# Performance work log

Hardware: AMD Instinct MI355X
Metric: run time of the kernel (lower is better)

Reference implementation:

```python
import jax, jax.numpy as jnp
import numpy as np

HEADS = 16
NEG_INF = np.float32(-2**32 + 1)  # matches TF code's padding value


def setup_inputs() -> dict:
    key = jax.random.key(0)
    ks = jax.random.split(key, 11)
    B, S, D = 2, 2048, 1024
    mk = lambda k, shape: jax.random.normal(k, shape, dtype=jnp.float32)
    return {
        "query": mk(ks[0], (B, S, D)),
        "key":   mk(ks[1], (B, S, D)),
        "value": mk(ks[2], (B, S, D)),
        "Wq": mk(ks[3], (D, D)) * (1.0 / np.sqrt(D)), "bq": jnp.zeros((D,), jnp.float32),
        "Wk": mk(ks[4], (D, D)) * (1.0 / np.sqrt(D)), "bk": jnp.zeros((D,), jnp.float32),
        "Wv": mk(ks[5], (D, D)) * (1.0 / np.sqrt(D)), "bv": jnp.zeros((D,), jnp.float32),
        "Wo": mk(ks[6], (D, D)) * (1.0 / np.sqrt(D)), "bo": jnp.zeros((D,), jnp.float32),
    }


def reference(query, key, value, Wq, bq, Wk, bk, Wv, bv, Wo, bo):
    B, S, D = query.shape
    H = HEADS
    dh = D // H
    # QKV projections with relu (as in the original Dense(activation=relu))
    q = jax.nn.relu(query @ Wq + bq).reshape(B, S, H, dh)
    k = jax.nn.relu(key   @ Wk + bk).reshape(B, S, H, dh)
    v = jax.nn.relu(value @ Wv + bv).reshape(B, S, H, dh)
    # scaled dot-product attention; scale = sqrt(per-head key dim)
    scores = jnp.einsum("bqhd,bkhd->bhqk", q, k) / jnp.sqrt(jnp.float32(dh))
    # causal mask (masked=True path): zeros above the diagonal -> NEG_INF
    causal = jnp.tril(jnp.ones((S, S), dtype=jnp.float32))  # [S,S]
    scores = jnp.where(causal == 0, NEG_INF, scores)
    attn = jax.nn.softmax(scores, axis=-1)  # [B,H,S,S]
    out = jnp.einsum("bhqk,bkhd->bqhd", attn, v).reshape(B, S, D)
    return jax.nn.relu(out @ Wo + bo)
```

## Files before the change

### kernel.cpp

```cpp
#include <hip/hip_runtime.h>
#include <hip/hip_bf16.h>

using bf16 = __hip_bfloat16;
typedef __attribute__((ext_vector_type(8))) short bf16x8;
typedef __attribute__((ext_vector_type(4))) float f32x4;

#define DEV __device__ __forceinline__

DEV float exp2fast(float x) { return __builtin_amdgcn_exp2f(x); }

DEV void gload_lds16(const void* g, void* l) {
  __builtin_amdgcn_global_load_lds((const __attribute__((address_space(1))) void*)g,
                                   (__attribute__((address_space(3))) void*)l, 16, 0, 0);
}

DEV unsigned pk2(float lo, float hi) {
  union { bf16 h[2]; unsigned u; } z;
  z.h[0] = __float2bfloat16(lo);
  z.h[1] = __float2bfloat16(hi);
  return z.u;
}

struct PrepArgs {
  const float* x[3]; bf16* y[3];
  const float* W[4]; bf16* WT[4];
};

__global__ __launch_bounds__(256) void prep_kernel(PrepArgs a) {
  __shared__ float tile[32][33];
  const int b = blockIdx.x;
  if (b < 6144) {
    const int which = b >> 11, blk = b & 2047;
    const int i = blk * 256 + threadIdx.x;
    const float4* xv = (const float4*)a.x[which];
    float4 p = xv[i * 2];
    float4 q = xv[i * 2 + 1];
    union { bf16 h[8]; uint4 v; } u;
    u.h[0] = __float2bfloat16(p.x); u.h[1] = __float2bfloat16(p.y);
    u.h[2] = __float2bfloat16(p.z); u.h[3] = __float2bfloat16(p.w);
    u.h[4] = __float2bfloat16(q.x); u.h[5] = __float2bfloat16(q.y);
    u.h[6] = __float2bfloat16(q.z); u.h[7] = __float2bfloat16(q.w);
    *(uint4*)&a.y[which][(size_t)i * 8] = u.v;
  } else {
    const int w = (b - 6144) >> 10, blk = (b - 6144) & 1023;
    const float* W = a.W[w];
    bf16* WT = a.WT[w];
    const int tx = threadIdx.x & 31, ty = threadIdx.x >> 5;
    const int n0 = (blk & 31) * 32, k0 = (blk >> 5) * 32;
#pragma unroll
    for (int i = ty; i < 32; i += 8)
      tile[i][tx] = W[(size_t)(k0 + i) * 1024 + n0 + tx];
    __syncthreads();
#pragma unroll
    for (int i = ty; i < 32; i += 8)
      WT[(size_t)(n0 + i) * 1024 + k0 + tx] = __float2bfloat16(tile[tx][i]);
  }
}

__global__ __launch_bounds__(256) void vtrans_kernel(const bf16* __restrict__ v,
                                                     bf16* __restrict__ VT) {
  __shared__ bf16 tile[64 * 64];
  const int t = threadIdx.x;
  const int bh = blockIdx.y, b = bh >> 4, h = bh & 15;
  const int s0 = blockIdx.x * 64;
  const int r0 = t >> 3, c8 = t & 7;
#pragma unroll
  for (int it = 0; it < 2; ++it) {
    int r = it * 32 + r0;
    uint4 d = *(const uint4*)&v[(size_t)(b * 2048 + s0 + r) * 1024 + h * 64 + c8 * 8];
    *(uint4*)&tile[r * 64 + ((c8 ^ (r >> 3)) * 8)] = d;
  }
  __syncthreads();
#pragma unroll
  for (int it = 0; it < 2; ++it) {
    int d = it * 32 + r0;
    int sc = c8 * 8;
    union { bf16 h[8]; uint4 v4; } u;
#pragma unroll
    for (int j = 0; j < 8; ++j) {
      int row = sc + j;
      u.h[j] = tile[row * 64 + (((d >> 3) ^ (row >> 3)) * 8) + (d & 7)];
    }
    *(uint4*)&VT[((size_t)bh * 64 + d) * 2048 + s0 + sc] = u.v4;
  }
}

template <int BM, typename OutT>
DEV void gemm_core(const bf16* __restrict__ A, const bf16* __restrict__ BT,
                   const float* __restrict__ bias, OutT* __restrict__ out) {
  constexpr int K = 1024, N = 1024;
  constexpr int MI = BM / 32;
  __shared__ bf16 ldsA[2][BM * 32];
  __shared__ bf16 ldsB[2][128 * 32];
  const int t = threadIdx.x;
  const int lane = t & 63, wid = t >> 6;
  const int wr = wid >> 1, wc = wid & 1;
  const int fr = lane & 15, fko = (lane >> 4) * 8;
  const size_t mBase = (size_t)blockIdx.y * BM;
  const size_t nBase = (size_t)blockIdx.x * 128;

  const int srow = t >> 2;
  const int scol = (t & 3) * 8;
  const bf16* gA = A + (mBase + srow) * K + scol;
  const bf16* gB = BT + (nBase + srow) * K + scol;
  const int ldst = wid * 512;

  f32x4 acc[MI][4];
#pragma unroll
  for (int i = 0; i < MI; ++i)
#pragma unroll
    for (int j = 0; j < 4; ++j) acc[i][j] = (f32x4){0.f, 0.f, 0.f, 0.f};

  gload_lds16(gA, &ldsA[0][ldst]);
  if constexpr (BM == 128) gload_lds16(gA + 64 * K, &ldsA[0][ldst + 2048]);
  gload_lds16(gB, &ldsB[0][ldst]);
  gload_lds16(gB + 64 * K, &ldsB[0][ldst + 2048]);
  __syncthreads();

  int buf = 0;
  for (int k0 = 0; k0 < K; k0 += 32) {
    if (k0 + 32 < K) {
      const int kn = k0 + 32;
      gload_lds16(gA + kn, &ldsA[buf ^ 1][ldst]);
      if constexpr (BM == 128) gload_lds16(gA + 64 * K + kn, &ldsA[buf ^ 1][ldst + 2048]);
      gload_lds16(gB + kn, &ldsB[buf ^ 1][ldst]);
      gload_lds16(gB + 64 * K + kn, &ldsB[buf ^ 1][ldst + 2048]);
    }
    bf16x8 aF[MI], bF[4];
#pragma unroll
    for (int i = 0; i < MI; ++i)
      aF[i] = *(const bf16x8*)&ldsA[buf][(wr * (BM / 2) + i * 16 + fr) * 32 + fko];
#pragma unroll
    for (int j = 0; j < 4; ++j)
      bF[j] = *(const bf16x8*)&ldsB[buf][(wc * 64 + j * 16 + fr) * 32 + fko];
#pragma unroll
    for (int i = 0; i < MI; ++i)
#pragma unroll
      for (int j = 0; j < 4; ++j)
        acc[i][j] = __builtin_amdgcn_mfma_f32_16x16x32_bf16(aF[i], bF[j], acc[i][j], 0, 0, 0);
    __syncthreads();
    buf ^= 1;
  }

  const int orow = (int)mBase + wr * (BM / 2) + (lane >> 4) * 4;
  const int ocol = (int)nBase + wc * 64 + fr;
#pragma unroll
  for (int j = 0; j < 4; ++j) {
    const float bj = bias[ocol + j * 16];
#pragma unroll
    for (int i = 0; i < MI; ++i)
#pragma unroll
      for (int r = 0; r < 4; ++r) {
        float v = fmaxf(acc[i][j][r] + bj, 0.f);
        size_t idx = (size_t)(orow + i * 16 + r) * N + (ocol + j * 16);
        if constexpr (sizeof(OutT) == 2) out[idx] = __float2bfloat16(v);
        else out[idx] = v;
      }
  }
}

struct QKVArgs {
  const bf16* A[3];
  const bf16* BT[3];
  const float* bias[3];
  bf16* out[3];
};

__global__ __launch_bounds__(256) void gemm_qkv_kernel(QKVArgs args) {
  const int z = blockIdx.z;
  gemm_core<128, bf16>(args.A[z], args.BT[z], args.bias[z], args.out[z]);
}

__global__ __launch_bounds__(256) void gemm_out_kernel(const bf16* __restrict__ A,
                                                       const bf16* __restrict__ BT,
                                                       const float* __restrict__ bias,
                                                       float* __restrict__ out) {
  gemm_core<64, float>(A, BT, bias, out);
}

__global__ __launch_bounds__(256, 2) void attn_kernel(const bf16* __restrict__ Qb,
                                                      const bf16* __restrict__ Kb,
                                                      const bf16* __restrict__ VTb,
                                                      bf16* __restrict__ Ob) {
  constexpr int Dm = 1024, S = 2048;
  __shared__ bf16 ldsK[2][128 * 64];
  __shared__ bf16 ldsV[2][64 * 128];
  const int t = threadIdx.x, l = t & 63, wid = t >> 6;

  const int lin = blockIdx.y * 16 + blockIdx.x;
  const int swz = (lin & 7) * 64 + (lin >> 3);
  const int bh = swz >> 4, pairp = swz & 15;
  const int b = bh >> 4, h = bh & 15;
  const int q4 = l & 15, fg = l >> 4;
  const bf16* Qg = Qb + (size_t)b * S * Dm + h * 64;
  const bf16* Kg = Kb + (size_t)b * S * Dm + h * 64;
  const bf16* VTg = VTb + (size_t)bh * 64 * S;

  const int krow0 = wid * 32 + (l >> 3);
  const int kch = ((l & 7) ^ (l >> 3)) * 8;
  const int vrl = l >> 4;
  const int vcb = l & 15;

  const int idx0 = ((q4 + ((l & 16) ? 32 : 0)) << 2);
  const int idx1 = idx0 + 64;

  constexpr float SC = 0.18033688f;

  auto STAGE = [&](int tile, int bi) {
    const int kvb = tile * 128;
#pragma unroll
    for (int g = 0; g < 4; ++g)
      gload_lds16(Kg + (size_t)(kvb + krow0 + 8 * g) * Dm + kch,
                  &ldsK[bi][(wid * 32 + 8 * g) * 64]);
#pragma unroll
    for (int g = 0; g < 4; ++g) {
      const int dr = wid * 16 + 4 * g + vrl;
      const int vch = (vcb ^ (4 * g + vrl)) * 8;
      gload_lds16(VTg + (size_t)dr * S + kvb + vch,
                  &ldsV[bi][(wid * 16 + 4 * g) * 128]);
    }
  };

#pragma unroll 1
  for (int ph = 0; ph < 2; ++ph) {
    const int qt = ph ? (31 - pairp) : pairp;
    const int qb = qt * 64;
    const int qw = qb + wid * 16;

    bf16x8 qF[2];
#pragma unroll
    for (int kd = 0; kd < 2; ++kd)
      qF[kd] = *(const bf16x8*)&Qg[(size_t)(qw + q4) * Dm + kd * 32 + fg * 8];

    f32x4 oacc[4];
#pragma unroll
    for (int n = 0; n < 4; ++n) oacc[n] = (f32x4){0.f, 0.f, 0.f, 0.f};
    float mrow = -3.0e38f, lsum = 0.f;

    const int nTiles = (qt + 2) >> 1;

    STAGE(0, 0);
    __syncthreads();

    int buf = 0;
    for (int tile = 0; tile < nTiles; ++tile) {
      const int kvb = tile * 128;
      if (tile + 1 < nTiles) STAGE(tile + 1, buf ^ 1);
      const bf16* kb = &ldsK[buf][0];
      const bf16* vb = &ldsV[buf][0];

      f32x4 sT[8];
#pragma unroll
      for (int n = 0; n < 8; ++n) sT[n] = (f32x4){0.f, 0.f, 0.f, 0.f};
      __builtin_amdgcn_s_setprio(1);
#pragma unroll
      for (int n = 0; n < 8; ++n) {
#pragma unroll
        for (int kd = 0; kd < 2; ++kd) {
          bf16x8 kf = *(const bf16x8*)&kb[(n * 16 + q4) * 64 + (((kd * 4 + fg) ^ (q4 & 7)) * 8)];
          sT[n] = __builtin_amdgcn_mfma_f32_16x16x32_bf16(kf, qF[kd], sT[n], 0, 0, 0);
        }
      }
      __builtin_amdgcn_s_setprio(0);

      const bool needmask = (tile == nTiles - 1);
      const int qrow = qw + q4;
#pragma unroll
      for (int n = 0; n < 8; ++n)
#pragma unroll
        for (int r = 0; r < 4; ++r) {
          float vv = sT[n][r] * SC;
          if (needmask) {
            int kv = kvb + n * 16 + fg * 4 + r;
            if (kv > qrow) vv = -1e30f;
          }
          sT[n][r] = vv;
        }
      float vm[8];
#pragma unroll
      for (int n = 0; n < 8; ++n)
        vm[n] = fmaxf(fmaxf(sT[n][0], sT[n][1]), fmaxf(sT[n][2], sT[n][3]));
      float tmax = fmaxf(fmaxf(fmaxf(vm[0], vm[1]), fmaxf(vm[2], vm[3])),
                         fmaxf(fmaxf(vm[4], vm[5]), fmaxf(vm[6], vm[7])));
      tmax = fmaxf(tmax, __shfl_xor(tmax, 16, 64));
      tmax = fmaxf(tmax, __shfl_xor(tmax, 32, 64));
      if (__any(tmax > mrow + 8.f)) {
        const float mnew = fmaxf(mrow, tmax);
        const float corr = exp2fast(mrow - mnew);
        mrow = mnew;
        lsum *= corr;
#pragma unroll
        for (int n = 0; n < 4; ++n)
#pragma unroll
          for (int r = 0; r < 4; ++r) oacc[n][r] *= corr;
      }
      float rv[8];
#pragma unroll
      for (int n = 0; n < 8; ++n) {
#pragma unroll
        for (int r = 0; r < 4; ++r) sT[n][r] = exp2fast(sT[n][r] - mrow);
        rv[n] = (sT[n][0] + sT[n][1]) + (sT[n][2] + sT[n][3]);
      }
      float rs = ((rv[0] + rv[1]) + (rv[2] + rv[3])) + ((rv[4] + rv[5]) + (rv[6] + rv[7]));
      rs += __shfl_xor(rs, 16, 64);
      rs += __shfl_xor(rs, 32, 64);
      lsum += rs;

#pragma unroll
      for (int ks = 0; ks < 4; ++ks) {
        const unsigned X0 = pk2(sT[2 * ks][0], sT[2 * ks][1]);
        const unsigned X1 = pk2(sT[2 * ks][2], sT[2 * ks][3]);
        const unsigned Y0 = pk2(sT[2 * ks + 1][0], sT[2 * ks + 1][1]);
        const unsigned Y1 = pk2(sT[2 * ks + 1][2], sT[2 * ks + 1][3]);
        union { int u[4]; bf16x8 v; } bfr;
        int zx, zy;
        zx = __builtin_amdgcn_ds_bpermute(idx0, (int)X0);
        zy = __builtin_amdgcn_ds_bpermute(idx0, (int)Y0);
        bfr.u[0] = (l & 32) ? zy : zx;
        zx = __builtin_amdgcn_ds_bpermute(idx0, (int)X1);
        zy = __builtin_amdgcn_ds_bpermute(idx0, (int)Y1);
        bfr.u[1] = (l & 32) ? zy : zx;
        zx = __builtin_amdgcn_ds_bpermute(idx1, (int)X0);
        zy = __builtin_amdgcn_ds_bpermute(idx1, (int)Y0);
        bfr.u[2] = (l & 32) ? zy : zx;
        zx = __builtin_amdgcn_ds_bpermute(idx1, (int)X1);
        zy = __builtin_amdgcn_ds_bpermute(idx1, (int)Y1);
        bfr.u[3] = (l & 32) ? zy : zx;
        __builtin_amdgcn_s_setprio(1);
#pragma unroll
        for (int dblk = 0; dblk < 4; ++dblk) {
          bf16x8 vf = *(const bf16x8*)&vb[(dblk * 16 + q4) * 128 + (((ks * 4 + fg) ^ q4) * 8)];
          oacc[dblk] = __builtin_amdgcn_mfma_f32_16x16x32_bf16(vf, bfr.v, oacc[dblk], 0, 0, 0);
        }
        __builtin_amdgcn_s_setprio(0);
      }
      __syncthreads();
      buf ^= 1;
    }

    bf16* ldsT = &ldsK[0][0] + wid * 1152;
    const float inv = 1.f / lsum;
#pragma unroll
    for (int dblk = 0; dblk < 4; ++dblk)
#pragma unroll
      for (int r = 0; r < 4; ++r) {
        int d = dblk * 16 + fg * 4 + r;
        ldsT[q4 * 72 + d] = __float2bfloat16(oacc[dblk][r] * inv);
      }
    asm volatile("s_waitcnt lgkmcnt(0)" ::: "memory");
    __builtin_amdgcn_sched_barrier(0);
    const int rq = l >> 2, dq = (l & 3) * 16;
#pragma unroll
    for (int i = 0; i < 2; ++i) {
      uint4 w = *(const uint4*)&ldsT[rq * 72 + dq + 8 * i];
      *(uint4*)&Ob[((size_t)b * S + qw + rq) * Dm + h * 64 + dq + 8 * i] = w;
    }
    __syncthreads();
  }
}

extern "C" void kernel_launch(void* const* d_in, const int* in_sizes, int n_in,
                              void* d_out, int out_size, void* d_ws, size_t ws_size,
                              hipStream_t stream) {
  const float* query = (const float*)d_in[0];
  const float* key   = (const float*)d_in[1];
  const float* value = (const float*)d_in[2];
  const float* Wq = (const float*)d_in[3]; const float* bq = (const float*)d_in[4];
  const float* Wk = (const float*)d_in[5]; const float* bk = (const float*)d_in[6];
  const float* Wv = (const float*)d_in[7]; const float* bv = (const float*)d_in[8];
  const float* Wo = (const float*)d_in[9]; const float* bo = (const float*)d_in[10];
  float* out = (float*)d_out;

  char* ws = (char*)d_ws;
  const size_t MB = 1024 * 1024;
  bf16* xq  = (bf16*)(ws + 0 * MB);
  bf16* xk  = (bf16*)(ws + 8 * MB);
  bf16* xv  = (bf16*)(ws + 16 * MB);
  bf16* qp  = (bf16*)(ws + 24 * MB);
  bf16* kp  = (bf16*)(ws + 32 * MB);
  bf16* vp  = (bf16*)(ws + 40 * MB);
  bf16* WqT = (bf16*)(ws + 48 * MB);
  bf16* WkT = (bf16*)(ws + 50 * MB);
  bf16* WvT = (bf16*)(ws + 52 * MB);
  bf16* WoT = (bf16*)(ws + 54 * MB);
  bf16* VT   = xq;
  bf16* attn = xk;

  PrepArgs pa;
  pa.x[0] = query; pa.x[1] = key; pa.x[2] = value;
  pa.y[0] = xq; pa.y[1] = xk; pa.y[2] = xv;
  pa.W[0] = Wq; pa.W[1] = Wk; pa.W[2] = Wv; pa.W[3] = Wo;
  pa.WT[0] = WqT; pa.WT[1] = WkT; pa.WT[2] = WvT; pa.WT[3] = WoT;
  prep_kernel<<<10240, 256, 0, stream>>>(pa);

  QKVArgs qa;
  qa.A[0] = xq;  qa.A[1] = xk;  qa.A[2] = xv;
  qa.BT[0] = WqT; qa.BT[1] = WkT; qa.BT[2] = WvT;
  qa.bias[0] = bq; qa.bias[1] = bk; qa.bias[2] = bv;
  qa.out[0] = qp; qa.out[1] = kp; qa.out[2] = vp;
  gemm_qkv_kernel<<<dim3(8, 32, 3), 256, 0, stream>>>(qa);

  vtrans_kernel<<<dim3(32, 32), 256, 0, stream>>>(vp, VT);
  attn_kernel<<<dim3(16, 32), 256, 0, stream>>>(qp, kp, VT, attn);
  gemm_out_kernel<<<dim3(8, 64), 256, 0, stream>>>(attn, WoT, bo, out);
}
```

Baseline: 235.9 us.

## Split long causal attention rows into two KV chunks with combine kernel

Replaces the paired-qtile causal scheduling with a split-KV scheme: q-tiles 16..31 are split into two KV chunks processed by separate blocks that write unnormalized partial outputs plus row max/sum, and a new combine kernel merges them. KV tiles shrink from 128 to 64, which cuts LDS use and allows four blocks per CU. The aim is better load balance and occupancy across 1536 blocks, at the cost of an extra kernel launch, partial-output traffic, and bf16 rounding of unnormalized partials.

```diff
diff --git a/kernel.cpp b/kernel.cpp
--- a/kernel.cpp
+++ b/kernel.cpp
@@ -178,184 +178,222 @@
   gemm_core<64, float>(A, BT, bias, out);
 }
 
-__global__ __launch_bounds__(256, 2) void attn_kernel(const bf16* __restrict__ Qb,
+__global__ __launch_bounds__(256, 4) void attn_kernel(const bf16* __restrict__ Qb,
                                                       const bf16* __restrict__ Kb,
                                                       const bf16* __restrict__ VTb,
-                                                      bf16* __restrict__ Ob) {
+                                                      bf16* __restrict__ Ob,
+                                                      bf16* __restrict__ pO,
+                                                      float* __restrict__ pm,
+                                                      float* __restrict__ pl) {
   constexpr int Dm = 1024, S = 2048;
-  __shared__ bf16 ldsK[2][128 * 64];
-  __shared__ bf16 ldsV[2][64 * 128];
+  __shared__ bf16 ldsK[2][4096];
+  __shared__ bf16 ldsV[2][4096];
   const int t = threadIdx.x, l = t & 63, wid = t >> 6;
 
-  const int lin = blockIdx.y * 16 + blockIdx.x;
-  const int swz = (lin & 7) * 64 + (lin >> 3);
-  const int bh = swz >> 4, pairp = swz & 15;
+  const int lin = blockIdx.y * 48 + blockIdx.x;
+  const int swz = (lin & 7) * 192 + (lin >> 3);
+  const int bh = swz / 48, cidx = swz % 48;
+  int qt, c0;
+  if (cidx < 16)      { qt = 16 + cidx;        c0 = 0; }
+  else if (cidx < 32) { qt = 31 - (cidx - 16); c0 = 1; }
+  else                { qt = 47 - cidx;        c0 = 0; }
+  const int t0 = c0 * 16;
+  const int t1 = (c0 == 0 && qt >= 16) ? 16 : (qt + 1);
+  const bool two_chunk = (qt >= 16);
+
   const int b = bh >> 4, h = bh & 15;
   const int q4 = l & 15, fg = l >> 4;
+  const int qw = qt * 64 + wid * 16;
   const bf16* Qg = Qb + (size_t)b * S * Dm + h * 64;
   const bf16* Kg = Kb + (size_t)b * S * Dm + h * 64;
   const bf16* VTg = VTb + (size_t)bh * 64 * S;
 
-  const int krow0 = wid * 32 + (l >> 3);
-  const int kch = ((l & 7) ^ (l >> 3)) * 8;
-  const int vrl = l >> 4;
-  const int vcb = l & 15;
+  const int srow = l >> 3;
+  const int schunk = (l & 7) ^ srow;
+  const bf16* kSrc = Kg + (size_t)(wid * 16 + srow) * Dm + schunk * 8;
+  const bf16* vSrc = VTg + (size_t)(wid * 16 + srow) * S + schunk * 8;
 
   const int idx0 = ((q4 + ((l & 16) ? 32 : 0)) << 2);
   const int idx1 = idx0 + 64;
-
   constexpr float SC = 0.18033688f;
 
+  bf16x8 qF[2];
+#pragma unroll
+  for (int kd = 0; kd < 2; ++kd)
+    qF[kd] = *(const bf16x8*)&Qg[(size_t)(qw + q4) * Dm + kd * 32 + fg * 8];
+
+  f32x4 oacc[4];
+#pragma unroll
+  for (int n = 0; n < 4; ++n) oacc[n] = (f32x4){0.f, 0.f, 0.f, 0.f};
+  float mrow = -3.0e38f, lsum = 0.f;
+
   auto STAGE = [&](int tile, int bi) {
-    const int kvb = tile * 128;
-#pragma unroll
-    for (int g = 0; g < 4; ++g)
-      gload_lds16(Kg + (size_t)(kvb + krow0 + 8 * g) * Dm + kch,
-                  &ldsK[bi][(wid * 32 + 8 * g) * 64]);
-#pragma unroll
-    for (int g = 0; g < 4; ++g) {
-      const int dr = wid * 16 + 4 * g + vrl;
-      const int vch = (vcb ^ (4 * g + vrl)) * 8;
-      gload_lds16(VTg + (size_t)dr * S + kvb + vch,
-                  &ldsV[bi][(wid * 16 + 4 * g) * 128]);
-    }
+    const size_t kvb = (size_t)tile * 64;
+    gload_lds16(kSrc + kvb * Dm, &ldsK[bi][wid * 1024]);
+    gload_lds16(kSrc + (kvb + 8) * Dm, &ldsK[bi][wid * 1024 + 512]);
+    gload_lds16(vSrc + kvb, &ldsV[bi][wid * 1024]);
+    gload_lds16(vSrc + kvb + 8 * S, &ldsV[bi][wid * 1024 + 512]);
   };
 
-#pragma unroll 1
-  for (int ph = 0; ph < 2; ++ph) {
-    const int qt = ph ? (31 - pairp) : pairp;
-    const int qb = qt * 64;
-    const int qw = qb + wid * 16;
-
-    bf16x8 qF[2];
-#pragma unroll
-    for (int kd = 0; kd < 2; ++kd)
-      qF[kd] = *(const bf16x8*)&Qg[(size_t)(qw + q4) * Dm + kd * 32 + fg * 8];
-
-    f32x4 oacc[4];
-#pragma unroll
-    for (int n = 0; n < 4; ++n) oacc[n] = (f32x4){0.f, 0.f, 0.f, 0.f};
-    float mrow = -3.0e38f, lsum = 0.f;
-
-    const int nTiles = (qt + 2) >> 1;
-
-    STAGE(0, 0);
-    __syncthreads();
-
-    int buf = 0;
-    for (int tile = 0; tile < nTiles; ++tile) {
-      const int kvb = tile * 128;
-      if (tile + 1 < nTiles) STAGE(tile + 1, buf ^ 1);
-      const bf16* kb = &ldsK[buf][0];
-      const bf16* vb = &ldsV[buf][0];
-
-      f32x4 sT[8];
-#pragma unroll
-      for (int n = 0; n < 8; ++n) sT[n] = (f32x4){0.f, 0.f, 0.f, 0.f};
+  STAGE(t0, 0);
+  __syncthreads();
+
+  int buf = 0;
+  for (int tile = t0; tile < t1; ++tile) {
+    if (tile + 1 < t1) STAGE(tile + 1, buf ^ 1);
+    const bf16* kb = &ldsK[buf][0];
+    const bf16* vb = &ldsV[buf][0];
+
+    f32x4 sT[4];
+#pragma unroll
+    for (int n = 0; n < 4; ++n) sT[n] = (f32x4){0.f, 0.f, 0.f, 0.f};
+    __builtin_amdgcn_s_setprio(1);
+#pragma unroll
+    for (int n = 0; n < 4; ++n) {
+#pragma unroll
+      for (int kd = 0; kd < 2; ++kd) {
+        bf16x8 kf = *(const bf16x8*)&kb[(n * 16 + q4) * 64 + (((kd * 4 + fg) ^ (q4 & 7)) * 8)];
+        sT[n] = __builtin_amdgcn_mfma_f32_16x16x32_bf16(kf, qF[kd], sT[n], 0, 0, 0);
+      }
+    }
+    __builtin_amdgcn_s_setprio(0);
+
+    const bool needmask = (tile == qt);
+    const int kvb = tile * 64, qrow = qw + q4;
+#pragma unroll
+    for (int n = 0; n < 4; ++n)
+#pragma unroll
+      for (int r = 0; r < 4; ++r) {
+        float vv = sT[n][r] * SC;
+        if (needmask) {
+          int kv = kvb + n * 16 + fg * 4 + r;
+          if (kv > qrow) vv = -1e30f;
+        }
+        sT[n][r] = vv;
+      }
+    float vm[4];
+#pragma unroll
+    for (int n = 0; n < 4; ++n)
+      vm[n] = fmaxf(fmaxf(sT[n][0], sT[n][1]), fmaxf(sT[n][2], sT[n][3]));
+    float tmax = fmaxf(fmaxf(vm[0], vm[1]), fmaxf(vm[2], vm[3]));
+    tmax = fmaxf(tmax, __shfl_xor(tmax, 16, 64));
+    tmax = fmaxf(tmax, __shfl_xor(tmax, 32, 64));
+    if (__any(tmax > mrow + 8.f)) {
+      const float mnew = fmaxf(mrow, tmax);
+      const float corr = exp2fast(mrow - mnew);
+      mrow = mnew;
+      lsum *= corr;
+#pragma unroll
+      for (int n = 0; n < 4; ++n)
+#pragma unroll
+        for (int r = 0; r < 4; ++r) oacc[n][r] *= corr;
+    }
+    float rv[4];
+#pragma unroll
+    for (int n = 0; n < 4; ++n) {
+#pragma unroll
+      for (int r = 0; r < 4; ++r) sT[n][r] = exp2fast(sT[n][r] - mrow);
+      rv[n] = (sT[n][0] + sT[n][1]) + (sT[n][2] + sT[n][3]);
+    }
+    float rs = (rv[0] + rv[1]) + (rv[2] + rv[3]);
+    rs += __shfl_xor(rs, 16, 64);
+    rs += __shfl_xor(rs, 32, 64);
+    lsum += rs;
+
+#pragma unroll
+    for (int ks = 0; ks < 2; ++ks) {
+      const unsigned X0 = pk2(sT[2 * ks][0], sT[2 * ks][1]);
+      const unsigned X1 = pk2(sT[2 * ks][2], sT[2 * ks][3]);
+      const unsigned Y0 = pk2(sT[2 * ks + 1][0], sT[2 * ks + 1][1]);
+      const unsigned Y1 = pk2(sT[2 * ks + 1][2], sT[2 * ks + 1][3]);
+      union { int u[4]; bf16x8 v; } bfr;
+      int zx, zy;
+      zx = __builtin_amdgcn_ds_bpermute(idx0, (int)X0);
+      zy = __builtin_amdgcn_ds_bpermute(idx0, (int)Y0);
+      bfr.u[0] = (l & 32) ? zy : zx;
+      zx = __builtin_amdgcn_ds_bpermute(idx0, (int)X1);
+      zy = __builtin_amdgcn_ds_bpermute(idx0, (int)Y1);
+      bfr.u[1] = (l & 32) ? zy : zx;
+      zx = __builtin_amdgcn_ds_bpermute(idx1, (int)X0);
+      zy = __builtin_amdgcn_ds_bpermute(idx1, (int)Y0);
+      bfr.u[2] = (l & 32) ? zy : zx;
+      zx = __builtin_amdgcn_ds_bpermute(idx1, (int)X1);
+      zy = __builtin_amdgcn_ds_bpermute(idx1, (int)Y1);
+      bfr.u[3] = (l & 32) ? zy : zx;
       __builtin_amdgcn_s_setprio(1);
 #pragma unroll
-      for (int n = 0; n < 8; ++n) {
-#pragma unroll
-        for (int kd = 0; kd < 2; ++kd) {
-          bf16x8 kf = *(const bf16x8*)&kb[(n * 16 + q4) * 64 + (((kd * 4 + fg) ^ (q4 & 7)) * 8)];
-          sT[n] = __builtin_amdgcn_mfma_f32_16x16x32_bf16(kf, qF[kd], sT[n], 0, 0, 0);
-        }
+      for (int dblk = 0; dblk < 4; ++dblk) {
+        bf16x8 vf = *(const bf16x8*)&vb[(dblk * 16 + q4) * 64 + (((ks * 4 + fg) ^ (q4 & 7)) * 8)];
+        oacc[dblk] = __builtin_amdgcn_mfma_f32_16x16x32_bf16(vf, bfr.v, oacc[dblk], 0, 0, 0);
       }
       __builtin_amdgcn_s_setprio(0);
-
-      const bool needmask = (tile == nTiles - 1);
-      const int qrow = qw + q4;
-#pragma unroll
-      for (int n = 0; n < 8; ++n)
-#pragma unroll
-        for (int r = 0; r < 4; ++r) {
-          float vv = sT[n][r] * SC;
-          if (needmask) {
-            int kv = kvb + n * 16 + fg * 4 + r;
-            if (kv > qrow) vv = -1e30f;
-          }
-          sT[n][r] = vv;
-        }
-      float vm[8];
-#pragma unroll
-      for (int n = 0; n < 8; ++n)
-        vm[n] = fmaxf(fmaxf(sT[n][0], sT[n][1]), fmaxf(sT[n][2], sT[n][3]));
-      float tmax = fmaxf(fmaxf(fmaxf(vm[0], vm[1]), fmaxf(vm[2], vm[3])),
-                         fmaxf(fmaxf(vm[4], vm[5]), fmaxf(vm[6], vm[7])));
-      tmax = fmaxf(tmax, __shfl_xor(tmax, 16, 64));
-      tmax = fmaxf(tmax, __shfl_xor(tmax, 32, 64));
-      if (__any(tmax > mrow + 8.f)) {
-        const float mnew = fmaxf(mrow, tmax);
-        const float corr = exp2fast(mrow - mnew);
-        mrow = mnew;
-        lsum *= corr;
-#pragma unroll
-        for (int n = 0; n < 4; ++n)
-#pragma unroll
-          for (int r = 0; r < 4; ++r) oacc[n][r] *= corr;
-      }
-      float rv[8];
-#pragma unroll
-      for (int n = 0; n < 8; ++n) {
-#pragma unroll
-        for (int r = 0; r < 4; ++r) sT[n][r] = exp2fast(sT[n][r] - mrow);
-        rv[n] = (sT[n][0] + sT[n][1]) + (sT[n][2] + sT[n][3]);
-      }
-      float rs = ((rv[0] + rv[1]) + (rv[2] + rv[3])) + ((rv[4] + rv[5]) + (rv[6] + rv[7]));
-      rs += __shfl_xor(rs, 16, 64);
-      rs += __shfl_xor(rs, 32, 64);
-      lsum += rs;
-
-#pragma unroll
-      for (int ks = 0; ks < 4; ++ks) {
-        const unsigned X0 = pk2(sT[2 * ks][0], sT[2 * ks][1]);
-        const unsigned X1 = pk2(sT[2 * ks][2], sT[2 * ks][3]);
-        const unsigned Y0 = pk2(sT[2 * ks + 1][0], sT[2 * ks + 1][1]);
-        const unsigned Y1 = pk2(sT[2 * ks + 1][2], sT[2 * ks + 1][3]);
-        union { int u[4]; bf16x8 v; } bfr;
-        int zx, zy;
-        zx = __builtin_amdgcn_ds_bpermute(idx0, (int)X0);
-        zy = __builtin_amdgcn_ds_bpermute(idx0, (int)Y0);
-        bfr.u[0] = (l & 32) ? zy : zx;
-        zx = __builtin_amdgcn_ds_bpermute(idx0, (int)X1);
-        zy = __builtin_amdgcn_ds_bpermute(idx0, (int)Y1);
-        bfr.u[1] = (l & 32) ? zy : zx;
-        zx = __builtin_amdgcn_ds_bpermute(idx1, (int)X0);
-        zy = __builtin_amdgcn_ds_bpermute(idx1, (int)Y0);
-        bfr.u[2] = (l & 32) ? zy : zx;
-        zx = __builtin_amdgcn_ds_bpermute(idx1, (int)X1);
-        zy = __builtin_amdgcn_ds_bpermute(idx1, (int)Y1);
-        bfr.u[3] = (l & 32) ? zy : zx;
-        __builtin_amdgcn_s_setprio(1);
-#pragma unroll
-        for (int dblk = 0; dblk < 4; ++dblk) {
-          bf16x8 vf = *(const bf16x8*)&vb[(dblk * 16 + q4) * 128 + (((ks * 4 + fg) ^ q4) * 8)];
-          oacc[dblk] = __builtin_amdgcn_mfma_f32_16x16x32_bf16(vf, bfr.v, oacc[dblk], 0, 0, 0);
-        }
-        __builtin_amdgcn_s_setprio(0);
-      }
-      __syncthreads();
-      buf ^= 1;
-    }
-
-    bf16* ldsT = &ldsK[0][0] + wid * 1152;
-    const float inv = 1.f / lsum;
-#pragma unroll
-    for (int dblk = 0; dblk < 4; ++dblk)
-#pragma unroll
-      for (int r = 0; r < 4; ++r) {
-        int d = dblk * 16 + fg * 4 + r;
-        ldsT[q4 * 72 + d] = __float2bfloat16(oacc[dblk][r] * inv);
-      }
-    asm volatile("s_waitcnt lgkmcnt(0)" ::: "memory");
-    __builtin_amdgcn_sched_barrier(0);
-    const int rq = l >> 2, dq = (l & 3) * 16;
+    }
+    __syncthreads();
+    buf ^= 1;
+  }
+
+  bf16* ldsT = &ldsK[0][0] + wid * 1152;
+  const float sc = two_chunk ? 1.f : (1.f / lsum);
+#pragma unroll
+  for (int dblk = 0; dblk < 4; ++dblk)
+#pragma unroll
+    for (int r = 0; r < 4; ++r) {
+      int d = dblk * 16 + fg * 4 + r;
+      ldsT[q4 * 72 + d] = __float2bfloat16(oacc[dblk][r] * sc);
+    }
+  asm volatile("s_waitcnt lgkmcnt(0)" ::: "memory");
+  __builtin_amdgcn_sched_barrier(0);
+  const int rq = l >> 2, dq = (l & 3) * 16;
+  if (two_chunk) {
+    const int slot = (bh * 16 + (qt - 16)) * 2 + c0;
+    bf16* pb = pO + (size_t)slot * 4096;
+#pragma unroll
+    for (int i = 0; i < 2; ++i) {
+      uint4 w = *(const uint4*)&ldsT[rq * 72 + dq + 8 * i];
+      *(uint4*)&pb[(wid * 16 + rq) * 64 + dq + 8 * i] = w;
+    }
+    if (l < 16) {
+      pm[slot * 64 + wid * 16 + l] = mrow;
+      pl[slot * 64 + wid * 16 + l] = lsum;
+    }
+  } else {
 #pragma unroll
     for (int i = 0; i < 2; ++i) {
       uint4 w = *(const uint4*)&ldsT[rq * 72 + dq + 8 * i];
       *(uint4*)&Ob[((size_t)b * S + qw + rq) * Dm + h * 64 + dq + 8 * i] = w;
     }
-    __syncthreads();
+  }
+}
+
+__global__ __launch_bounds__(256) void combine_kernel(const bf16* __restrict__ pO,
+                                                      const float* __restrict__ pm,
+                                                      const float* __restrict__ pl,
+                                                      bf16* __restrict__ Ob) {
+  constexpr int Dm = 1024, S = 2048;
+  const int qt = 16 + blockIdx.x, bh = blockIdx.y;
+  const int b = bh >> 4, h = bh & 15;
+  const int t = threadIdx.x;
+  const int row = t >> 2, dg = (t & 3) * 16;
+  const int slot0 = (bh * 16 + (qt - 16)) * 2;
+  const float m0 = pm[slot0 * 64 + row], m1 = pm[(slot0 + 1) * 64 + row];
+  const float l0 = pl[slot0 * 64 + row], l1 = pl[(slot0 + 1) * 64 + row];
+  const float M = fmaxf(m0, m1);
+  const float w0 = exp2fast(m0 - M), w1 = exp2fast(m1 - M);
+  const float L = w0 * l0 + w1 * l1;
+  const float s0 = w0 / L, s1 = w1 / L;
+  const bf16* p0 = pO + (size_t)slot0 * 4096 + row * 64 + dg;
+  const bf16* p1 = p0 + 4096;
+  bf16* dst = Ob + ((size_t)b * S + qt * 64 + row) * Dm + h * 64 + dg;
+#pragma unroll
+  for (int i = 0; i < 2; ++i) {
+    union { bf16 h8[8]; uint4 v; } a0, a1, o;
+    a0.v = *(const uint4*)&p0[8 * i];
+    a1.v = *(const uint4*)&p1[8 * i];
+#pragma unroll
+    for (int j = 0; j < 8; ++j)
+      o.h8[j] = __float2bfloat16(s0 * __bfloat162float(a0.h8[j]) +
+                                 s1 * __bfloat162float(a1.h8[j]));
+    *(uint4*)&dst[8 * i] = o.v;
   }
 }
 
@@ -383,8 +421,11 @@
   bf16* WkT = (bf16*)(ws + 50 * MB);
   bf16* WvT = (bf16*)(ws + 52 * MB);
   bf16* WoT = (bf16*)(ws + 54 * MB);
-  bf16* VT   = xq;
-  bf16* attn = xk;
+  bf16*  VT    = xq;
+  bf16*  pO    = xk;
+  float* pm    = (float*)(ws + 16 * MB);
+  float* pl    = (float*)(ws + 17 * MB);
+  bf16*  attnO = vp;
 
   PrepArgs pa;
   pa.x[0] = query; pa.x[1] = key; pa.x[2] = value;
@@ -401,6 +442,7 @@
   gemm_qkv_kernel<<<dim3(8, 32, 3), 256, 0, stream>>>(qa);
 
   vtrans_kernel<<<dim3(32, 32), 256, 0, stream>>>(vp, VT);
-  attn_kernel<<<dim3(16, 32), 256, 0, stream>>>(qp, kp, VT, attn);
-  gemm_out_kernel<<<dim3(8, 64), 256, 0, stream>>>(attn, WoT, bo, out);
-}
+  attn_kernel<<<dim3(48, 32), 256, 0, stream>>>(qp, kp, VT, attnO, pO, pm, pl);
+  combine_kernel<<<dim3(16, 32), 256, 0, stream>>>(pO, pm, pl, attnO);
+  gemm_out_kernel<<<dim3(8, 64), 256, 0, stream>>>(attnO, WoT, bo, out);
+}
```

After: 244.0 us. +3.4%, slower.
